# Optimization experiments

Measured on AMD Instinct MI355X. Metric: run time of the kernel, lower is better.

## Reference

```python
import jax, jax.numpy as jnp
import numpy as np

NUM_MODELS = 4
B = 16384
HIDDEN = 512
QDIM = 256
LAST_HIDDEN = 256
UW = 0.1          # uncertainty_weight
EPS = 1e-5        # LayerNorm eps (torch default)
FEAT_DIMS = [1024, 768, 512, 640]


def _linear(x, W, b):
    return x @ W.T + b


def _layernorm(h, g, b):
    mu = jnp.mean(h, axis=-1, keepdims=True)
    var = jnp.mean((h - mu) ** 2, axis=-1, keepdims=True)
    return (h - mu) * jax.lax.rsqrt(var + EPS) * g + b


def setup_inputs() -> dict:
    key = jax.random.key(0)
    ks = jax.random.split(key, 40)
    inp = {}
    for i, d in enumerate(FEAT_DIMS):
        inp[f"feat{i}"] = jax.random.normal(ks[i], (B, d), jnp.float32)
        inp[f"W_intra{i}"] = jax.random.normal(ks[4 + i], (HIDDEN, d), jnp.float32) / np.sqrt(d)
        inp[f"b_intra{i}"] = jnp.zeros((HIDDEN,), jnp.float32)
    inp["pred_scores"] = jax.random.uniform(ks[8], (B, NUM_MODELS), jnp.float32)
    inp["pred_vars"] = jax.random.uniform(ks[9], (B, NUM_MODELS), jnp.float32)
    inp["ln_g"] = jnp.ones((HIDDEN,), jnp.float32)
    inp["ln_b"] = jnp.zeros((HIDDEN,), jnp.float32)
    inp["Wq"] = jax.random.normal(ks[10], (QDIM, HIDDEN), jnp.float32) / np.sqrt(HIDDEN)
    inp["bq"] = jnp.zeros((QDIM,), jnp.float32)
    inp["Wk"] = jax.random.normal(ks[11], (QDIM, HIDDEN), jnp.float32) / np.sqrt(HIDDEN)
    inp["bk"] = jnp.zeros((QDIM,), jnp.float32)
    inp["Wv"] = jax.random.normal(ks[12], (QDIM, HIDDEN), jnp.float32) / np.sqrt(HIDDEN)
    inp["bv"] = jnp.zeros((QDIM,), jnp.float32)
    d1 = NUM_MODELS * QDIM + NUM_MODELS
    inp["W1"] = jax.random.normal(ks[13], (LAST_HIDDEN, d1), jnp.float32) / np.sqrt(d1)
    inp["b1"] = jnp.zeros((LAST_HIDDEN,), jnp.float32)
    inp["Wfc"] = jax.random.normal(ks[14], (1, LAST_HIDDEN), jnp.float32) / np.sqrt(LAST_HIDDEN)
    inp["bfc"] = jnp.zeros((1,), jnp.float32)
    return inp


def _forward(feats, pred_scores, pred_vars, W_intras, b_intras,
             ln_g, ln_b, Wq, bq, Wk, bk, Wv, bv, W1, b1, Wfc, bfc):
    # per-model branch: Linear -> ReLU -> (dropout=id) -> ReLU -> LayerNorm
    hiddens = []
    for i in range(NUM_MODELS):
        h = jax.nn.relu(_linear(feats[i], W_intras[i], b_intras[i]))
        h = jax.nn.relu(h)  # second relu after dropout (identity in eval)
        hiddens.append(_layernorm(h, ln_g, ln_b))
    H = jnp.stack(hiddens, axis=1)  # (B, M, HIDDEN)

    # cross-attention with uncertainty; NOTE source bug: key = drop(q) => keys == queries
    q = jnp.einsum('bmh,qh->bmq', H, Wq) + bq          # (B, M, Q)
    k = q                                              # faithful to `key = self.drop(q)`
    v = jnp.einsum('bmh,qh->bmq', H, Wv) + bv          # (B, M, Q)

    scores = jnp.einsum('biq,bjq->bij', q, k)          # (B, M, M)
    vars_ = pred_vars[:, None, :] + pred_vars[:, :, None]  # vars[b,i,j] = v[b,j] + v[b,i]
    scores = jax.nn.softmax(scores - UW * vars_, axis=-1)
    z = jnp.einsum('bij,bjq->biq', scores, v).reshape(B, NUM_MODELS * QDIM)

    out = jnp.concatenate([z, pred_scores], axis=-1)
    out = _linear(out, W1, b1)
    logits = _linear(out, Wfc, bfc)
    return jax.nn.sigmoid(logits)  # (B, 1)


def reference(feat0, feat1, feat2, feat3,
              W_intra0, b_intra0, W_intra1, b_intra1,
              W_intra2, b_intra2, W_intra3, b_intra3,
              pred_scores, pred_vars, ln_g, ln_b,
              Wq, bq, Wk, bk, Wv, bv, W1, b1, Wfc, bfc):
    feats = [feat0, feat1, feat2, feat3]
    W_intras = [W_intra0, W_intra1, W_intra2, W_intra3]
    b_intras = [b_intra0, b_intra1, b_intra2, b_intra3]
    return _forward(feats, pred_scores, pred_vars, W_intras, b_intras,
                    ln_g, ln_b, Wq, bq, Wk, bk, Wv, bv, W1, b1, Wfc, bfc)
```

## Files before the change

kernel.cpp:

```cpp
#include <hip/hip_runtime.h>
#include <hip/hip_bf16.h>


typedef __bf16 bf16;
typedef __bf16 bf16x4_t __attribute__((ext_vector_type(4)));
typedef __bf16 bf16x8_t __attribute__((ext_vector_type(8)));
typedef float  f32x4_t  __attribute__((ext_vector_type(4)));

__device__ __forceinline__ bf16x8_t cvt8(f32x4_t a, f32x4_t b) {
  bf16x8_t r;
  r[0] = (bf16)a[0]; r[1] = (bf16)a[1]; r[2] = (bf16)a[2]; r[3] = (bf16)a[3];
  r[4] = (bf16)b[0]; r[5] = (bf16)b[1]; r[6] = (bf16)b[2]; r[7] = (bf16)b[3];
  return r;
}

__device__ __forceinline__ void gl_lds16(const void* g, void* l) {
  __builtin_amdgcn_global_load_lds(
      (const __attribute__((address_space(1))) void*)g,
      (__attribute__((address_space(3))) void*)l, 16, 0, 0);
}

__device__ __forceinline__ bf16x8_t frag_read(const bf16* Ts, int row, int c0) {
  const int byte = row * 64 + ((c0 ^ ((row >> 1) & 3)) << 4);
  return *(const bf16x8_t*)((const char*)Ts + byte);
}

__device__ __forceinline__ void stage_b16(const bf16* __restrict__ src, int ld,
                                          int k0, bf16* lds) {
  const int l = threadIdx.x & 63;
  const int w = threadIdx.x >> 6;
#pragma unroll
  for (int j = 0; j < 2; ++j) {
    const int rb = w * 32 + j * 16;
    const int r  = rb + (l >> 2);
    const int sc = (l & 3) ^ ((r >> 1) & 3);
    gl_lds16(src + (size_t)r * ld + k0 + sc * 8, (char*)lds + rb * 64);
  }
}

__device__ __forceinline__ void commit2(const f32x4_t v[4], bf16* lds,
                                        int srow, int shalf) {
  const int sw = (srow >> 1) & 3;
  *(bf16x8_t*)((char*)lds + srow * 64 + (((shalf * 2)     ^ sw) << 4)) = cvt8(v[0], v[1]);
  *(bf16x8_t*)((char*)lds + srow * 64 + (((shalf * 2 + 1) ^ sw) << 4)) = cvt8(v[2], v[3]);
}

__device__ __forceinline__ void mfma_step(const bf16* As, const bf16* Bs,
                                          f32x4_t acc[4][4]) {
  const int lane = threadIdx.x & 63;
  const int wid  = threadIdx.x >> 6;
  const int wm = wid >> 1, wn = wid & 1;
  const int fr = lane & 15, c0 = lane >> 4;
  bf16x8_t ar[4], br[4];
#pragma unroll
  for (int mi = 0; mi < 4; ++mi) ar[mi] = frag_read(As, wm * 64 + mi * 16 + fr, c0);
#pragma unroll
  for (int ni = 0; ni < 4; ++ni) br[ni] = frag_read(Bs, wn * 64 + ni * 16 + fr, c0);
#pragma unroll
  for (int mi = 0; mi < 4; ++mi)
#pragma unroll
    for (int ni = 0; ni < 4; ++ni)
      acc[mi][ni] = __builtin_amdgcn_mfma_f32_16x16x32_bf16(ar[mi], br[ni], acc[mi][ni], 0, 0, 0);
}

#define WAIT_VM6()  asm volatile("s_waitcnt vmcnt(6)" ::: "memory")
#define WAIT_VM0()  asm volatile("s_waitcnt vmcnt(0)" ::: "memory")
#define WAIT_LGKM() asm volatile("s_waitcnt lgkmcnt(0)" ::: "memory")
#define SBAR()      __builtin_amdgcn_s_barrier()
#define SCHED0()    __builtin_amdgcn_sched_barrier(0)

template<int REG_IS_A>
__device__ __forceinline__ void core_db(
    const float* __restrict__ regsrc, int rld,
    const bf16* __restrict__ dmasrc, int dld, int K,
    bf16* R0, bf16* R1, bf16* D0, bf16* D1, f32x4_t acc[4][4])
{
  const int tid  = threadIdx.x;
  const int srow = tid >> 1, shalf = tid & 1;
  const float* Rf = regsrc + (size_t)srow * rld + shalf * 16;

  f32x4_t ra[4], rb[4];
#pragma unroll
  for (int i = 0; i < 4; ++i) ra[i] = *(const f32x4_t*)(Rf + i * 4);
  stage_b16(dmasrc, dld, 0, D0);

  for (int k0 = 0; k0 < K; k0 += 64) {
    stage_b16(dmasrc, dld, k0 + 32, D1);
#pragma unroll
    for (int i = 0; i < 4; ++i) rb[i] = *(const f32x4_t*)(Rf + k0 + 32 + i * 4);
    WAIT_VM6();
    commit2(ra, R0, srow, shalf);
    WAIT_LGKM();
    SBAR(); SCHED0();
    if (REG_IS_A) mfma_step(R0, D0, acc); else mfma_step(D0, R0, acc);
    SCHED0(); SBAR();
    if (k0 + 64 < K) {
      stage_b16(dmasrc, dld, k0 + 64, D0);
#pragma unroll
      for (int i = 0; i < 4; ++i) ra[i] = *(const f32x4_t*)(Rf + k0 + 64 + i * 4);
      WAIT_VM6();
    } else {
      WAIT_VM0();
    }
    commit2(rb, R1, srow, shalf);
    WAIT_LGKM();
    SBAR(); SCHED0();
    if (REG_IS_A) mfma_step(R1, D1, acc); else mfma_step(D1, R1, acc);
    SCHED0(); SBAR();
  }
}

template<int RELU>
__device__ __forceinline__ void epi_bf16(f32x4_t acc[4][4], bf16* __restrict__ C, int ldc,
                                         const float* __restrict__ bias) {
  const int lane = threadIdx.x & 63;
  const int wid  = threadIdx.x >> 6;
  const int wm = wid >> 1, wn = wid & 1;
  const int fr = lane & 15;
  const int rb = wm * 64 + 4 * (lane >> 4);
  const int cb = wn * 64 + fr;
  float bv[4];
#pragma unroll
  for (int ni = 0; ni < 4; ++ni) bv[ni] = bias[cb + ni * 16];
#pragma unroll
  for (int mi = 0; mi < 4; ++mi)
#pragma unroll
    for (int j = 0; j < 4; ++j)
#pragma unroll
      for (int ni = 0; ni < 4; ++ni) {
        float val = acc[mi][ni][j] + bv[ni];
        if (RELU) val = fmaxf(val, 0.f);
        C[(size_t)(rb + mi * 16 + j) * ldc + cb + ni * 16] = (bf16)val;
      }
}

__device__ __forceinline__ void cp8(bf16* d, const float* s) {
  f32x4_t x0 = *(const f32x4_t*)s;
  f32x4_t x1 = *(const f32x4_t*)(s + 4);
  *(bf16x8_t*)d = cvt8(x0, x1);
}

__global__ __launch_bounds__(256) void prep_kernel(
    const float* __restrict__ w0, const float* __restrict__ w1s,
    const float* __restrict__ w2, const float* __restrict__ w3,
    bf16* __restrict__ o0, bf16* __restrict__ o1,
    bf16* __restrict__ o2, bf16* __restrict__ o3) {
  const int t = blockIdx.x * 256 + threadIdx.x;
  if (t < 65536)       { size_t i = (size_t)t * 8;            cp8(o0 + i, w0 + i); }
  else if (t < 114688) { size_t i = (size_t)(t - 65536) * 8;  cp8(o1 + i, w1s + i); }
  else if (t < 147456) { size_t i = (size_t)(t - 114688) * 8; cp8(o2 + i, w2 + i); }
  else                 { size_t i = (size_t)(t - 147456) * 8; cp8(o3 + i, w3 + i); }
}

__global__ __launch_bounds__(256) void intra_kernel(
    const float* __restrict__ f0, const float* __restrict__ f1,
    const float* __restrict__ f2, const float* __restrict__ f3,
    const bf16* __restrict__ wb0, const bf16* __restrict__ wb1,
    const bf16* __restrict__ wb2, const bf16* __restrict__ wb3,
    const float* __restrict__ bb0, const float* __restrict__ bb1,
    const float* __restrict__ bb2, const float* __restrict__ bb3,
    bf16* __restrict__ hbuf) {
  __shared__ bf16 A0[128 * 32], A1[128 * 32], B0[128 * 32], B1[128 * 32];
  const int bid = blockIdx.x;
  const int lid = (bid & 7) * 256 + (bid >> 3);
  const int x = lid & 3;
  const int g = lid >> 2;
  const int z = g & 3;
  const int y = g >> 2;
  const float* fp; const bf16* wp; const float* bp; int K;
  switch (z) {
    case 0:  fp = f0; wp = wb0; bp = bb0; K = 1024; break;
    case 1:  fp = f1; wp = wb1; bp = bb1; K = 768;  break;
    case 2:  fp = f2; wp = wb2; bp = bb2; K = 512;  break;
    default: fp = f3; wp = wb3; bp = bb3; K = 640;  break;
  }
  f32x4_t acc[4][4];
#pragma unroll
  for (int i = 0; i < 4; ++i)
#pragma unroll
    for (int j = 0; j < 4; ++j) acc[i][j] = (f32x4_t){0.f, 0.f, 0.f, 0.f};
  core_db<1>(fp + (size_t)(y * 128) * K, K,
             wp + (size_t)(x * 128) * K, K, K, A0, A1, B0, B1, acc);
  bf16* C = hbuf + (size_t)(y * 128) * 2048 + z * 512 + x * 128;
  epi_bf16<1>(acc, C, 2048, bp + x * 128);
}

__global__ __launch_bounds__(256) void qv_kernel(
    const bf16* __restrict__ H, const float* __restrict__ Wq,
    const float* __restrict__ Wv, const float* __restrict__ bq,
    const float* __restrict__ bv, bf16* __restrict__ qvout) {
  __shared__ bf16 A0[128 * 32], A1[128 * 32], B0[128 * 32], B1[128 * 32];
  const int bid = blockIdx.x;
  const int lid = (bid & 7) * 256 + (bid >> 3);
  const int x = lid & 3, y = lid >> 2;
  const float* Wsrc = (x < 2) ? Wq : Wv;
  f32x4_t acc[4][4];
#pragma unroll
  for (int i = 0; i < 4; ++i)
#pragma unroll
    for (int j = 0; j < 4; ++j) acc[i][j] = (f32x4_t){0.f, 0.f, 0.f, 0.f};
  core_db<0>(Wsrc + (size_t)((x & 1) * 128) * 512, 512,
             H + (size_t)(y * 128) * 512, 512, 512, B0, B1, A0, A1, acc);
  const float* bias = (x < 2) ? bq + x * 128 : bv + (x - 2) * 128;
  epi_bf16<0>(acc, qvout + (size_t)(y * 128) * 512 + x * 128, 512, bias);
}

__global__ __launch_bounds__(256) void w1_kernel(
    const bf16* __restrict__ zb, const float* __restrict__ W1,
    const float* __restrict__ b1, const float* __restrict__ ps,
    float* __restrict__ obuf) {
  __shared__ bf16 A0[128 * 32], A1[128 * 32], B0[128 * 32], B1[128 * 32];
  const int bid = blockIdx.x;
  const int lid = (bid & 7) * 32 + (bid >> 3);
  const int x = lid & 1, y = lid >> 1;
  f32x4_t acc[4][4];
#pragma unroll
  for (int i = 0; i < 4; ++i)
#pragma unroll
    for (int j = 0; j < 4; ++j) acc[i][j] = (f32x4_t){0.f, 0.f, 0.f, 0.f};
  core_db<0>(W1 + (size_t)(x * 128) * 1028, 1028,
             zb + (size_t)(y * 128) * 1024, 1024, 1024, B0, B1, A0, A1, acc);

  const int lane = threadIdx.x & 63;
  const int wid  = threadIdx.x >> 6;
  const int wm = wid >> 1, wn = wid & 1;
  const int fr = lane & 15;
  const int rb = wm * 64 + 4 * (lane >> 4);
  const int cb = x * 128 + wn * 64 + fr;
  float bv[4], wt[4][4];
#pragma unroll
  for (int ni = 0; ni < 4; ++ni) {
    bv[ni] = b1[cb + ni * 16];
#pragma unroll
    for (int m = 0; m < 4; ++m) wt[ni][m] = W1[(size_t)(cb + ni * 16) * 1028 + 1024 + m];
  }
#pragma unroll
  for (int mi = 0; mi < 4; ++mi)
#pragma unroll
    for (int j = 0; j < 4; ++j) {
      const int r = y * 128 + rb + mi * 16 + j;
      f32x4_t psv = *(const f32x4_t*)(ps + (size_t)r * 4);
#pragma unroll
      for (int ni = 0; ni < 4; ++ni) {
        float val = acc[mi][ni][j] + bv[ni]
                  + psv[0] * wt[ni][0] + psv[1] * wt[ni][1]
                  + psv[2] * wt[ni][2] + psv[3] * wt[ni][3];
        obuf[(size_t)r * 256 + cb + ni * 16] = val;
      }
    }
}

__global__ __launch_bounds__(256)
void ln_kernel(bf16* __restrict__ h, const float* __restrict__ g,
               const float* __restrict__ bta) {
  const int row  = blockIdx.x * 4 + (threadIdx.x >> 6);
  const int lane = threadIdx.x & 63;
  bf16* p = h + (size_t)row * 512 + lane * 8;
  const bf16x8_t x = *(const bf16x8_t*)p;
  float xf[8]; float s = 0.f, s2 = 0.f;
#pragma unroll
  for (int j = 0; j < 8; ++j) { xf[j] = (float)x[j]; s += xf[j]; s2 += xf[j] * xf[j]; }
#pragma unroll
  for (int off = 1; off < 64; off <<= 1) { s += __shfl_xor(s, off); s2 += __shfl_xor(s2, off); }
  const float mu  = s * (1.f / 512.f);
  const float var = s2 * (1.f / 512.f) - mu * mu;
  const float inv = rsqrtf(var + 1e-5f);
  f32x4_t g0 = *(const f32x4_t*)(g + lane * 8);
  f32x4_t g1 = *(const f32x4_t*)(g + lane * 8 + 4);
  f32x4_t b0 = *(const f32x4_t*)(bta + lane * 8);
  f32x4_t b1 = *(const f32x4_t*)(bta + lane * 8 + 4);
  bf16x8_t o;
#pragma unroll
  for (int j = 0; j < 4; ++j) o[j]     = (bf16)((xf[j] - mu) * inv * g0[j] + b0[j]);
#pragma unroll
  for (int j = 0; j < 4; ++j) o[4 + j] = (bf16)((xf[4 + j] - mu) * inv * g1[j] + b1[j]);
  *(bf16x8_t*)p = o;
}

__global__ __launch_bounds__(256)
void attn_kernel(const bf16* __restrict__ qv, const float* __restrict__ pvars,
                 bf16* __restrict__ z) {
  const int b    = blockIdx.x * 4 + (threadIdx.x >> 6);
  const int lane = threadIdx.x & 63;
  float qf[4][4], vf[4][4];
#pragma unroll
  for (int i = 0; i < 4; ++i) {
    const bf16* row = qv + ((size_t)b * 4 + i) * 512;
    bf16x4_t qq = *(const bf16x4_t*)(row + lane * 4);
    bf16x4_t vv = *(const bf16x4_t*)(row + 256 + lane * 4);
#pragma unroll
    for (int c = 0; c < 4; ++c) { qf[i][c] = (float)qq[c]; vf[i][c] = (float)vv[c]; }
  }
  float s[4][4];
#pragma unroll
  for (int i = 0; i < 4; ++i)
#pragma unroll
    for (int j = 0; j < 4; ++j)
      s[i][j] = qf[i][0] * qf[j][0] + qf[i][1] * qf[j][1] + qf[i][2] * qf[j][2] + qf[i][3] * qf[j][3];
#pragma unroll
  for (int off = 1; off < 64; off <<= 1)
#pragma unroll
    for (int i = 0; i < 4; ++i)
#pragma unroll
      for (int j = 0; j < 4; ++j) s[i][j] += __shfl_xor(s[i][j], off);

  float var4[4];
#pragma unroll
  for (int m = 0; m < 4; ++m) var4[m] = pvars[(size_t)b * 4 + m];
  float w[4][4];
#pragma unroll
  for (int i = 0; i < 4; ++i) {
    float t[4]; float mx = -1e30f;
#pragma unroll
    for (int j = 0; j < 4; ++j) { t[j] = s[i][j] - 0.1f * (var4[i] + var4[j]); mx = fmaxf(mx, t[j]); }
    float sum = 0.f;
#pragma unroll
    for (int j = 0; j < 4; ++j) { t[j] = expf(t[j] - mx); sum += t[j]; }
    const float is = 1.f / sum;
#pragma unroll
    for (int j = 0; j < 4; ++j) w[i][j] = t[j] * is;
  }
#pragma unroll
  for (int i = 0; i < 4; ++i) {
    bf16x4_t zo;
#pragma unroll
    for (int c = 0; c < 4; ++c) {
      float zf = w[i][0] * vf[0][c] + w[i][1] * vf[1][c] + w[i][2] * vf[2][c] + w[i][3] * vf[3][c];
      zo[c] = (bf16)zf;
    }
    *(bf16x4_t*)(z + ((size_t)b * 4 + i) * 256 + lane * 4) = zo;
  }
}

__global__ __launch_bounds__(256)
void fc_kernel(const float* __restrict__ o, const float* __restrict__ wfc,
               const float* __restrict__ bfc, float* __restrict__ out) {
  const int b    = blockIdx.x * 4 + (threadIdx.x >> 6);
  const int lane = threadIdx.x & 63;
  f32x4_t ov = *(const f32x4_t*)(o + (size_t)b * 256 + lane * 4);
  f32x4_t wv = *(const f32x4_t*)(wfc + lane * 4);
  float p = ov[0] * wv[0] + ov[1] * wv[1] + ov[2] * wv[2] + ov[3] * wv[3];
#pragma unroll
  for (int off = 1; off < 64; off <<= 1) p += __shfl_xor(p, off);
  if (lane == 0) {
    const float lg = p + bfc[0];
    out[b] = 1.f / (1.f + expf(-lg));
  }
}

extern "C" void kernel_launch(void* const* d_in, const int* in_sizes, int n_in,
                              void* d_out, int out_size, void* d_ws, size_t ws_size,
                              hipStream_t stream) {
  (void)in_sizes; (void)n_in; (void)out_size; (void)ws_size;
  const float* feat[4] = {(const float*)d_in[0], (const float*)d_in[3],
                          (const float*)d_in[6], (const float*)d_in[9]};
  const float* Wi[4]   = {(const float*)d_in[1], (const float*)d_in[4],
                          (const float*)d_in[7], (const float*)d_in[10]};
  const float* bi[4]   = {(const float*)d_in[2], (const float*)d_in[5],
                          (const float*)d_in[8], (const float*)d_in[11]};
  const float* ps  = (const float*)d_in[12];
  const float* pv  = (const float*)d_in[13];
  const float* lng = (const float*)d_in[14];
  const float* lnb = (const float*)d_in[15];
  const float* Wq  = (const float*)d_in[16];
  const float* bq  = (const float*)d_in[17];
  const float* Wv  = (const float*)d_in[20];
  const float* bvp = (const float*)d_in[21];
  const float* W1  = (const float*)d_in[22];
  const float* b1  = (const float*)d_in[23];
  const float* Wfc = (const float*)d_in[24];
  const float* bfc = (const float*)d_in[25];

  char* ws = (char*)d_ws;
  const size_t MB = 1024 * 1024;
  bf16*  hbuf  = (bf16*)ws;
  bf16*  zbuf  = (bf16*)ws;
  float* obuf  = (float*)(ws + 32 * MB);
  bf16*  wb0   = (bf16*)(ws + 64 * MB);
  bf16*  wb1   = (bf16*)(ws + 65 * MB);
  bf16*  wb2   = (bf16*)(ws + 65 * MB + 786432);
  bf16*  wb3   = (bf16*)(ws + 66 * MB + 262144);
  bf16*  qvout = (bf16*)(ws + 64 * MB);

  hipLaunchKernelGGL(prep_kernel, dim3(736), dim3(256), 0, stream,
                     Wi[0], Wi[1], Wi[2], Wi[3], wb0, wb1, wb2, wb3);
  hipLaunchKernelGGL(intra_kernel, dim3(2048), dim3(256), 0, stream,
                     feat[0], feat[1], feat[2], feat[3],
                     wb0, wb1, wb2, wb3, bi[0], bi[1], bi[2], bi[3], hbuf);
  hipLaunchKernelGGL(ln_kernel, dim3(65536 / 4), dim3(256), 0, stream, hbuf, lng, lnb);
  hipLaunchKernelGGL(qv_kernel, dim3(2048), dim3(256), 0, stream,
                     hbuf, Wq, Wv, bq, bvp, qvout);
  hipLaunchKernelGGL(attn_kernel, dim3(16384 / 4), dim3(256), 0, stream, qvout, pv, zbuf);
  hipLaunchKernelGGL(w1_kernel, dim3(256), dim3(256), 0, stream, zbuf, W1, b1, ps, obuf);
  hipLaunchKernelGGL(fc_kernel, dim3(16384 / 4), dim3(256), 0, stream, obuf, Wfc, bfc, (float*)d_out);
}
```

Baseline: 279.4 us.

## Fuse LayerNorm into per-model intra GEMM with full-row 64x512 tiles

Reshapes the intra-branch GEMM so each block computes a 64-row by full 512-column tile, with each warp covering 128 columns. This lets bias, ReLU and LayerNorm be applied in LDS right after the GEMM, so the separate ln_kernel launch and its read-modify-write pass over the hidden buffer go away. The cost is a much larger LDS footprint (72KB), more accumulator registers per thread, and halved grid size, which lowers occupancy and latency hiding.

```diff
diff --git a/kernel.cpp b/kernel.cpp
--- a/kernel.cpp
+++ b/kernel.cpp
@@ -38,6 +38,19 @@
   }
 }
 
+__device__ __forceinline__ void stage_b512(const bf16* __restrict__ src, int ld,
+                                           int k0, bf16* lds) {
+  const int l = threadIdx.x & 63;
+  const int w = threadIdx.x >> 6;
+#pragma unroll
+  for (int j = 0; j < 8; ++j) {
+    const int rb = w * 128 + j * 16;
+    const int r  = rb + (l >> 2);
+    const int sc = (l & 3) ^ ((r >> 1) & 3);
+    gl_lds16(src + (size_t)r * ld + k0 + sc * 8, (char*)lds + rb * 64);
+  }
+}
+
 __device__ __forceinline__ void commit2(const f32x4_t v[4], bf16* lds,
                                         int srow, int shalf) {
   const int sw = (srow >> 1) & 3;
@@ -63,7 +76,25 @@
       acc[mi][ni] = __builtin_amdgcn_mfma_f32_16x16x32_bf16(ar[mi], br[ni], acc[mi][ni], 0, 0, 0);
 }
 
+__device__ __forceinline__ void mfma_step8(const bf16* As, const bf16* Bs,
+                                           f32x4_t acc[4][8]) {
+  const int lane = threadIdx.x & 63;
+  const int wn   = threadIdx.x >> 6;
+  const int fr = lane & 15, c0 = lane >> 4;
+  bf16x8_t ar[4], br[8];
+#pragma unroll
+  for (int mi = 0; mi < 4; ++mi) ar[mi] = frag_read(As, mi * 16 + fr, c0);
+#pragma unroll
+  for (int ni = 0; ni < 8; ++ni) br[ni] = frag_read(Bs, wn * 128 + ni * 16 + fr, c0);
+#pragma unroll
+  for (int mi = 0; mi < 4; ++mi)
+#pragma unroll
+    for (int ni = 0; ni < 8; ++ni)
+      acc[mi][ni] = __builtin_amdgcn_mfma_f32_16x16x32_bf16(ar[mi], br[ni], acc[mi][ni], 0, 0, 0);
+}
+
 #define WAIT_VM6()  asm volatile("s_waitcnt vmcnt(6)" ::: "memory")
+#define WAIT_VM10() asm volatile("s_waitcnt vmcnt(10)" ::: "memory")
 #define WAIT_VM0()  asm volatile("s_waitcnt vmcnt(0)" ::: "memory")
 #define WAIT_LGKM() asm volatile("s_waitcnt lgkmcnt(0)" ::: "memory")
 #define SBAR()      __builtin_amdgcn_s_barrier()
@@ -152,21 +183,26 @@
   else                 { size_t i = (size_t)(t - 147456) * 8; cp8(o3 + i, w3 + i); }
 }
 
-__global__ __launch_bounds__(256) void intra_kernel(
+__global__ __launch_bounds__(256, 2) void intra_ln_kernel(
     const float* __restrict__ f0, const float* __restrict__ f1,
     const float* __restrict__ f2, const float* __restrict__ f3,
     const bf16* __restrict__ wb0, const bf16* __restrict__ wb1,
     const bf16* __restrict__ wb2, const bf16* __restrict__ wb3,
     const float* __restrict__ bb0, const float* __restrict__ bb1,
     const float* __restrict__ bb2, const float* __restrict__ bb3,
-    bf16* __restrict__ hbuf) {
-  __shared__ bf16 A0[128 * 32], A1[128 * 32], B0[128 * 32], B1[128 * 32];
+    const float* __restrict__ lng, const float* __restrict__ lnb,
+    bf16* __restrict__ Hout) {
+  __shared__ __align__(16) char smem[73728];
+  bf16* B0 = (bf16*)smem;
+  bf16* B1 = (bf16*)(smem + 32768);
+  bf16* A0 = (bf16*)(smem + 65536);
+  bf16* A1 = (bf16*)(smem + 69632);
+  bf16* hl = (bf16*)smem;
+
   const int bid = blockIdx.x;
-  const int lid = (bid & 7) * 256 + (bid >> 3);
-  const int x = lid & 3;
-  const int g = lid >> 2;
-  const int z = g & 3;
-  const int y = g >> 2;
+  const int lid = (bid & 7) * 128 + (bid >> 3);
+  const int z = lid & 3;
+  const int y = lid >> 2;
   const float* fp; const bf16* wp; const float* bp; int K;
   switch (z) {
     case 0:  fp = f0; wp = wb0; bp = bb0; K = 1024; break;
@@ -174,15 +210,89 @@
     case 2:  fp = f2; wp = wb2; bp = bb2; K = 512;  break;
     default: fp = f3; wp = wb3; bp = bb3; K = 640;  break;
   }
-  f32x4_t acc[4][4];
+  const int tid  = threadIdx.x;
+  const int lane = tid & 63;
+  const int wn   = tid >> 6;
+  const int srow = tid >> 2, sq = tid & 3;
+  const float* Af = fp + (size_t)(y * 64 + srow) * K + sq * 8;
+  const int abyte = srow * 64 + ((sq ^ ((srow >> 1) & 3)) << 4);
+
+  f32x4_t acc[4][8];
 #pragma unroll
   for (int i = 0; i < 4; ++i)
 #pragma unroll
-    for (int j = 0; j < 4; ++j) acc[i][j] = (f32x4_t){0.f, 0.f, 0.f, 0.f};
-  core_db<1>(fp + (size_t)(y * 128) * K, K,
-             wp + (size_t)(x * 128) * K, K, K, A0, A1, B0, B1, acc);
-  bf16* C = hbuf + (size_t)(y * 128) * 2048 + z * 512 + x * 128;
-  epi_bf16<1>(acc, C, 2048, bp + x * 128);
+    for (int j = 0; j < 8; ++j) acc[i][j] = (f32x4_t){0.f, 0.f, 0.f, 0.f};
+
+  f32x4_t ra0, ra1, rb0, rb1;
+  ra0 = *(const f32x4_t*)(Af + 0);  ra1 = *(const f32x4_t*)(Af + 4);
+  stage_b512(wp, K, 0, B0);
+
+  for (int k0 = 0; k0 < K; k0 += 64) {
+    stage_b512(wp, K, k0 + 32, B1);
+    rb0 = *(const f32x4_t*)(Af + k0 + 32);  rb1 = *(const f32x4_t*)(Af + k0 + 36);
+    WAIT_VM10();
+    { f32x4_t v[1]; (void)v; }
+    *(bf16x8_t*)((char*)A0 + abyte) = cvt8(ra0, ra1);
+    WAIT_LGKM();
+    SBAR(); SCHED0();
+    mfma_step8(A0, B0, acc);
+    SCHED0(); SBAR();
+    if (k0 + 64 < K) {
+      stage_b512(wp, K, k0 + 64, B0);
+      ra0 = *(const f32x4_t*)(Af + k0 + 64);  ra1 = *(const f32x4_t*)(Af + k0 + 68);
+      WAIT_VM10();
+    } else {
+      WAIT_VM0();
+    }
+    *(bf16x8_t*)((char*)A1 + abyte) = cvt8(rb0, rb1);
+    WAIT_LGKM();
+    SBAR(); SCHED0();
+    mfma_step8(A1, B1, acc);
+    SCHED0(); SBAR();
+  }
+
+  const int fr = lane & 15;
+  const int rbase = 4 * (lane >> 4);
+  const int cb = wn * 128 + fr;
+  float bv[8];
+#pragma unroll
+  for (int ni = 0; ni < 8; ++ni) bv[ni] = bp[cb + ni * 16];
+#pragma unroll
+  for (int mi = 0; mi < 4; ++mi)
+#pragma unroll
+    for (int j = 0; j < 4; ++j) {
+      const int row = mi * 16 + rbase + j;
+#pragma unroll
+      for (int ni = 0; ni < 8; ++ni) {
+        float v = fmaxf(acc[mi][ni][j] + bv[ni], 0.f);
+        hl[row * 512 + cb + ni * 16] = (bf16)v;
+      }
+    }
+  __syncthreads();
+
+  f32x4_t g0 = *(const f32x4_t*)(lng + lane * 8);
+  f32x4_t g1 = *(const f32x4_t*)(lng + lane * 8 + 4);
+  f32x4_t be0 = *(const f32x4_t*)(lnb + lane * 8);
+  f32x4_t be1 = *(const f32x4_t*)(lnb + lane * 8 + 4);
+#pragma unroll
+  for (int r16 = 0; r16 < 16; ++r16) {
+    const int row = wn * 16 + r16;
+    const bf16x8_t xv = *(const bf16x8_t*)(hl + row * 512 + lane * 8);
+    float xf[8]; float s = 0.f, s2 = 0.f;
+#pragma unroll
+    for (int j = 0; j < 8; ++j) { xf[j] = (float)xv[j]; s += xf[j]; s2 += xf[j] * xf[j]; }
+#pragma unroll
+    for (int off = 1; off < 64; off <<= 1) { s += __shfl_xor(s, off); s2 += __shfl_xor(s2, off); }
+    const float mu  = s * (1.f / 512.f);
+    const float var = s2 * (1.f / 512.f) - mu * mu;
+    const float inv = rsqrtf(var + 1e-5f);
+    bf16x8_t o;
+#pragma unroll
+    for (int j = 0; j < 4; ++j) o[j]     = (bf16)((xf[j] - mu) * inv * g0[j] + be0[j]);
+#pragma unroll
+    for (int j = 0; j < 4; ++j) o[4 + j] = (bf16)((xf[4 + j] - mu) * inv * g1[j] + be1[j]);
+    *(bf16x8_t*)(Hout + (size_t)(y * 64 + row) * 2048 + z * 512 + lane * 8) = o;
+  }
 }
 
 __global__ __launch_bounds__(256) void qv_kernel(
@@ -248,33 +358,6 @@
         obuf[(size_t)r * 256 + cb + ni * 16] = val;
       }
     }
-}
-
-__global__ __launch_bounds__(256)
-void ln_kernel(bf16* __restrict__ h, const float* __restrict__ g,
-               const float* __restrict__ bta) {
-  const int row  = blockIdx.x * 4 + (threadIdx.x >> 6);
-  const int lane = threadIdx.x & 63;
-  bf16* p = h + (size_t)row * 512 + lane * 8;
-  const bf16x8_t x = *(const bf16x8_t*)p;
-  float xf[8]; float s = 0.f, s2 = 0.f;
-#pragma unroll
-  for (int j = 0; j < 8; ++j) { xf[j] = (float)x[j]; s += xf[j]; s2 += xf[j] * xf[j]; }
-#pragma unroll
-  for (int off = 1; off < 64; off <<= 1) { s += __shfl_xor(s, off); s2 += __shfl_xor(s2, off); }
-  const float mu  = s * (1.f / 512.f);
-  const float var = s2 * (1.f / 512.f) - mu * mu;
-  const float inv = rsqrtf(var + 1e-5f);
-  f32x4_t g0 = *(const f32x4_t*)(g + lane * 8);
-  f32x4_t g1 = *(const f32x4_t*)(g + lane * 8 + 4);
-  f32x4_t b0 = *(const f32x4_t*)(bta + lane * 8);
-  f32x4_t b1 = *(const f32x4_t*)(bta + lane * 8 + 4);
-  bf16x8_t o;
-#pragma unroll
-  for (int j = 0; j < 4; ++j) o[j]     = (bf16)((xf[j] - mu) * inv * g0[j] + b0[j]);
-#pragma unroll
-  for (int j = 0; j < 4; ++j) o[4 + j] = (bf16)((xf[4 + j] - mu) * inv * g1[j] + b1[j]);
-  *(bf16x8_t*)p = o;
 }
 
 __global__ __launch_bounds__(256)
@@ -373,7 +456,7 @@
 
   char* ws = (char*)d_ws;
   const size_t MB = 1024 * 1024;
-  bf16*  hbuf  = (bf16*)ws;
+  bf16*  Hbuf  = (bf16*)ws;
   bf16*  zbuf  = (bf16*)ws;
   float* obuf  = (float*)(ws + 32 * MB);
   bf16*  wb0   = (bf16*)(ws + 64 * MB);
@@ -384,12 +467,12 @@
 
   hipLaunchKernelGGL(prep_kernel, dim3(736), dim3(256), 0, stream,
                      Wi[0], Wi[1], Wi[2], Wi[3], wb0, wb1, wb2, wb3);
-  hipLaunchKernelGGL(intra_kernel, dim3(2048), dim3(256), 0, stream,
+  hipLaunchKernelGGL(intra_ln_kernel, dim3(1024), dim3(256), 0, stream,
                      feat[0], feat[1], feat[2], feat[3],
-                     wb0, wb1, wb2, wb3, bi[0], bi[1], bi[2], bi[3], hbuf);
-  hipLaunchKernelGGL(ln_kernel, dim3(65536 / 4), dim3(256), 0, stream, hbuf, lng, lnb);
+                     wb0, wb1, wb2, wb3, bi[0], bi[1], bi[2], bi[3],
+                     lng, lnb, Hbuf);
   hipLaunchKernelGGL(qv_kernel, dim3(2048), dim3(256), 0, stream,
-                     hbuf, Wq, Wv, bq, bvp, qvout);
+                     Hbuf, Wq, Wv, bq, bvp, qvout);
   hipLaunchKernelGGL(attn_kernel, dim3(16384 / 4), dim3(256), 0, stream, qvout, pv, zbuf);
   hipLaunchKernelGGL(w1_kernel, dim3(256), dim3(256), 0, stream, zbuf, W1, b1, ps, obuf);
   hipLaunchKernelGGL(fc_kernel, dim3(16384 / 4), dim3(256), 0, stream, obuf, Wfc, bfc, (float*)d_out);
```

Measured after the change: 255.4 us. 1.09x faster.

## Stage fp32 operands via LDS DMA with triple-buffered GEMM pipeline

Applied to the files above, without the earlier changes.

Replaces the register-staged fp32 operand path (global load to registers, convert, write to LDS) with direct global-to-LDS DMA of fp32 tiles in a swizzled layout. The fp32-to-bf16 conversion now happens at fragment-read time. The two-stage double buffer becomes a three-deep ring buffer with graded vmcnt waits and raised wave priority around the MFMA block, so more loads are in flight and VGPR staging is removed. This costs 72KB of LDS per block, which likely lowers occupancy to one or two blocks per CU, and doubles LDS read traffic for the fp32 operand.

```diff
diff --git a/kernel.cpp b/kernel.cpp
--- a/kernel.cpp
+++ b/kernel.cpp
@@ -20,11 +20,13 @@
       (__attribute__((address_space(3))) void*)l, 16, 0, 0);
 }
 
-__device__ __forceinline__ bf16x8_t frag_read(const bf16* Ts, int row, int c0) {
+#define SBAR()   __builtin_amdgcn_s_barrier()
+#define SCHED0() __builtin_amdgcn_sched_barrier(0)
+
+__device__ __forceinline__ bf16x8_t frag_b16(const bf16* Ts, int row, int c0) {
   const int byte = row * 64 + ((c0 ^ ((row >> 1) & 3)) << 4);
   return *(const bf16x8_t*)((const char*)Ts + byte);
 }
-
 __device__ __forceinline__ void stage_b16(const bf16* __restrict__ src, int ld,
                                           int k0, bf16* lds) {
   const int l = threadIdx.x & 63;
@@ -38,24 +40,60 @@
   }
 }
 
-__device__ __forceinline__ void commit2(const f32x4_t v[4], bf16* lds,
-                                        int srow, int shalf) {
-  const int sw = (srow >> 1) & 3;
-  *(bf16x8_t*)((char*)lds + srow * 64 + (((shalf * 2)     ^ sw) << 4)) = cvt8(v[0], v[1]);
-  *(bf16x8_t*)((char*)lds + srow * 64 + (((shalf * 2 + 1) ^ sw) << 4)) = cvt8(v[2], v[3]);
-}
-
-__device__ __forceinline__ void mfma_step(const bf16* As, const bf16* Bs,
-                                          f32x4_t acc[4][4]) {
+__device__ __forceinline__ bf16x8_t frag_f32(const float* Ts, int row, int g) {
+  const int p0 = (2 * g)     ^ (row & 7);
+  const int p1 = (2 * g + 1) ^ (row & 7);
+  f32x4_t lo = *(const f32x4_t*)((const char*)Ts + row * 128 + (p0 << 4));
+  f32x4_t hi = *(const f32x4_t*)((const char*)Ts + row * 128 + (p1 << 4));
+  return cvt8(lo, hi);
+}
+__device__ __forceinline__ void stage_f32(const float* __restrict__ src, int ld,
+                                          int k0, float* lds) {
+  const int l = threadIdx.x & 63;
+  const int w = threadIdx.x >> 6;
+#pragma unroll
+  for (int j = 0; j < 4; ++j) {
+    const int rb = w * 32 + j * 8;
+    const int r  = rb + (l >> 3);
+    const int q  = (l & 7) ^ (r & 7);
+    gl_lds16(src + (size_t)r * ld + k0 + q * 4, (char*)lds + rb * 128);
+  }
+}
+
+template<int AF32>
+__device__ __forceinline__ void stage_deep(const void* A, int lda, const void* B,
+                                           int ldb, int k0, char* buf) {
+  if (AF32) {
+    stage_f32((const float*)A, lda, k0, (float*)buf);
+    stage_b16((const bf16*)B, ldb, k0, (bf16*)(buf + 16384));
+  } else {
+    stage_b16((const bf16*)A, lda, k0, (bf16*)buf);
+    stage_f32((const float*)B, ldb, k0, (float*)(buf + 8192));
+  }
+}
+
+template<int AF32>
+__device__ __forceinline__ void mfma_deep(const char* buf, f32x4_t acc[4][4]) {
   const int lane = threadIdx.x & 63;
   const int wid  = threadIdx.x >> 6;
   const int wm = wid >> 1, wn = wid & 1;
-  const int fr = lane & 15, c0 = lane >> 4;
+  const int fr = lane & 15, g = lane >> 4;
   bf16x8_t ar[4], br[4];
-#pragma unroll
-  for (int mi = 0; mi < 4; ++mi) ar[mi] = frag_read(As, wm * 64 + mi * 16 + fr, c0);
-#pragma unroll
-  for (int ni = 0; ni < 4; ++ni) br[ni] = frag_read(Bs, wn * 64 + ni * 16 + fr, c0);
+  if (AF32) {
+    const float* Af = (const float*)buf;
+    const bf16*  Bb = (const bf16*)(buf + 16384);
+#pragma unroll
+    for (int mi = 0; mi < 4; ++mi) ar[mi] = frag_f32(Af, wm * 64 + mi * 16 + fr, g);
+#pragma unroll
+    for (int ni = 0; ni < 4; ++ni) br[ni] = frag_b16(Bb, wn * 64 + ni * 16 + fr, g);
+  } else {
+    const bf16*  Ab = (const bf16*)buf;
+    const float* Bf = (const float*)(buf + 8192);
+#pragma unroll
+    for (int mi = 0; mi < 4; ++mi) ar[mi] = frag_b16(Ab, wm * 64 + mi * 16 + fr, g);
+#pragma unroll
+    for (int ni = 0; ni < 4; ++ni) br[ni] = frag_f32(Bf, wn * 64 + ni * 16 + fr, g);
+  }
 #pragma unroll
   for (int mi = 0; mi < 4; ++mi)
 #pragma unroll
@@ -63,50 +101,27 @@
       acc[mi][ni] = __builtin_amdgcn_mfma_f32_16x16x32_bf16(ar[mi], br[ni], acc[mi][ni], 0, 0, 0);
 }
 
-#define WAIT_VM6()  asm volatile("s_waitcnt vmcnt(6)" ::: "memory")
-#define WAIT_VM0()  asm volatile("s_waitcnt vmcnt(0)" ::: "memory")
-#define WAIT_LGKM() asm volatile("s_waitcnt lgkmcnt(0)" ::: "memory")
-#define SBAR()      __builtin_amdgcn_s_barrier()
-#define SCHED0()    __builtin_amdgcn_sched_barrier(0)
-
-template<int REG_IS_A>
-__device__ __forceinline__ void core_db(
-    const float* __restrict__ regsrc, int rld,
-    const bf16* __restrict__ dmasrc, int dld, int K,
-    bf16* R0, bf16* R1, bf16* D0, bf16* D1, f32x4_t acc[4][4])
-{
-  const int tid  = threadIdx.x;
-  const int srow = tid >> 1, shalf = tid & 1;
-  const float* Rf = regsrc + (size_t)srow * rld + shalf * 16;
-
-  f32x4_t ra[4], rb[4];
-#pragma unroll
-  for (int i = 0; i < 4; ++i) ra[i] = *(const f32x4_t*)(Rf + i * 4);
-  stage_b16(dmasrc, dld, 0, D0);
-
-  for (int k0 = 0; k0 < K; k0 += 64) {
-    stage_b16(dmasrc, dld, k0 + 32, D1);
-#pragma unroll
-    for (int i = 0; i < 4; ++i) rb[i] = *(const f32x4_t*)(Rf + k0 + 32 + i * 4);
-    WAIT_VM6();
-    commit2(ra, R0, srow, shalf);
-    WAIT_LGKM();
+template<int AF32>
+__device__ __forceinline__ void core_deep3(const void* A, int lda, const void* B,
+                                           int ldb, int K, char* lds,
+                                           f32x4_t acc[4][4]) {
+  const int nt = K >> 5;
+  stage_deep<AF32>(A, lda, B, ldb, 0,  lds);
+  stage_deep<AF32>(A, lda, B, ldb, 32, lds + 24576);
+  stage_deep<AF32>(A, lda, B, ldb, 64, lds + 49152);
+  int buf = 0;
+  for (int t = 0; t < nt; ++t) {
+    const int ahead = nt - 1 - t;
+    if (ahead >= 2)      asm volatile("s_waitcnt vmcnt(12)" ::: "memory");
+    else if (ahead == 1) asm volatile("s_waitcnt vmcnt(6)"  ::: "memory");
+    else                 asm volatile("s_waitcnt vmcnt(0)"  ::: "memory");
     SBAR(); SCHED0();
-    if (REG_IS_A) mfma_step(R0, D0, acc); else mfma_step(D0, R0, acc);
+    __builtin_amdgcn_s_setprio(1);
+    mfma_deep<AF32>(lds + buf * 24576, acc);
+    __builtin_amdgcn_s_setprio(0);
     SCHED0(); SBAR();
-    if (k0 + 64 < K) {
-      stage_b16(dmasrc, dld, k0 + 64, D0);
-#pragma unroll
-      for (int i = 0; i < 4; ++i) ra[i] = *(const f32x4_t*)(Rf + k0 + 64 + i * 4);
-      WAIT_VM6();
-    } else {
-      WAIT_VM0();
-    }
-    commit2(rb, R1, srow, shalf);
-    WAIT_LGKM();
-    SBAR(); SCHED0();
-    if (REG_IS_A) mfma_step(R1, D1, acc); else mfma_step(D1, R1, acc);
-    SCHED0(); SBAR();
+    if (t + 3 < nt) stage_deep<AF32>(A, lda, B, ldb, (t + 3) * 32, lds + buf * 24576);
+    buf = (buf == 2) ? 0 : buf + 1;
   }
 }
 
@@ -160,7 +175,7 @@
     const float* __restrict__ bb0, const float* __restrict__ bb1,
     const float* __restrict__ bb2, const float* __restrict__ bb3,
     bf16* __restrict__ hbuf) {
-  __shared__ bf16 A0[128 * 32], A1[128 * 32], B0[128 * 32], B1[128 * 32];
+  __shared__ __align__(16) char lds[73728];
   const int bid = blockIdx.x;
   const int lid = (bid & 7) * 256 + (bid >> 3);
   const int x = lid & 3;
@@ -179,75 +194,10 @@
   for (int i = 0; i < 4; ++i)
 #pragma unroll
     for (int j = 0; j < 4; ++j) acc[i][j] = (f32x4_t){0.f, 0.f, 0.f, 0.f};
-  core_db<1>(fp + (size_t)(y * 128) * K, K,
-             wp + (size_t)(x * 128) * K, K, K, A0, A1, B0, B1, acc);
+  core_deep3<1>(fp + (size_t)(y * 128) * K, K,
+                wp + (size_t)(x * 128) * K, K, K, lds, acc);
   bf16* C = hbuf + (size_t)(y * 128) * 2048 + z * 512 + x * 128;
   epi_bf16<1>(acc, C, 2048, bp + x * 128);
-}
-
-__global__ __launch_bounds__(256) void qv_kernel(
-    const bf16* __restrict__ H, const float* __restrict__ Wq,
-    const float* __restrict__ Wv, const float* __restrict__ bq,
-    const float* __restrict__ bv, bf16* __restrict__ qvout) {
-  __shared__ bf16 A0[128 * 32], A1[128 * 32], B0[128 * 32], B1[128 * 32];
-  const int bid = blockIdx.x;
-  const int lid = (bid & 7) * 256 + (bid >> 3);
-  const int x = lid & 3, y = lid >> 2;
-  const float* Wsrc = (x < 2) ? Wq : Wv;
-  f32x4_t acc[4][4];
-#pragma unroll
-  for (int i = 0; i < 4; ++i)
-#pragma unroll
-    for (int j = 0; j < 4; ++j) acc[i][j] = (f32x4_t){0.f, 0.f, 0.f, 0.f};
-  core_db<0>(Wsrc + (size_t)((x & 1) * 128) * 512, 512,
-             H + (size_t)(y * 128) * 512, 512, 512, B0, B1, A0, A1, acc);
-  const float* bias = (x < 2) ? bq + x * 128 : bv + (x - 2) * 128;
-  epi_bf16<0>(acc, qvout + (size_t)(y * 128) * 512 + x * 128, 512, bias);
-}
-
-__global__ __launch_bounds__(256) void w1_kernel(
-    const bf16* __restrict__ zb, const float* __restrict__ W1,
-    const float* __restrict__ b1, const float* __restrict__ ps,
-    float* __restrict__ obuf) {
-  __shared__ bf16 A0[128 * 32], A1[128 * 32], B0[128 * 32], B1[128 * 32];
-  const int bid = blockIdx.x;
-  const int lid = (bid & 7) * 32 + (bid >> 3);
-  const int x = lid & 1, y = lid >> 1;
-  f32x4_t acc[4][4];
-#pragma unroll
-  for (int i = 0; i < 4; ++i)
-#pragma unroll
-    for (int j = 0; j < 4; ++j) acc[i][j] = (f32x4_t){0.f, 0.f, 0.f, 0.f};
-  core_db<0>(W1 + (size_t)(x * 128) * 1028, 1028,
-             zb + (size_t)(y * 128) * 1024, 1024, 1024, B0, B1, A0, A1, acc);
-
-  const int lane = threadIdx.x & 63;
-  const int wid  = threadIdx.x >> 6;
-  const int wm = wid >> 1, wn = wid & 1;
-  const int fr = lane & 15;
-  const int rb = wm * 64 + 4 * (lane >> 4);
-  const int cb = x * 128 + wn * 64 + fr;
-  float bv[4], wt[4][4];
-#pragma unroll
-  for (int ni = 0; ni < 4; ++ni) {
-    bv[ni] = b1[cb + ni * 16];
-#pragma unroll
-    for (int m = 0; m < 4; ++m) wt[ni][m] = W1[(size_t)(cb + ni * 16) * 1028 + 1024 + m];
-  }
-#pragma unroll
-  for (int mi = 0; mi < 4; ++mi)
-#pragma unroll
-    for (int j = 0; j < 4; ++j) {
-      const int r = y * 128 + rb + mi * 16 + j;
-      f32x4_t psv = *(const f32x4_t*)(ps + (size_t)r * 4);
-#pragma unroll
-      for (int ni = 0; ni < 4; ++ni) {
-        float val = acc[mi][ni][j] + bv[ni]
-                  + psv[0] * wt[ni][0] + psv[1] * wt[ni][1]
-                  + psv[2] * wt[ni][2] + psv[3] * wt[ni][3];
-        obuf[(size_t)r * 256 + cb + ni * 16] = val;
-      }
-    }
 }
 
 __global__ __launch_bounds__(256)
@@ -275,6 +225,71 @@
 #pragma unroll
   for (int j = 0; j < 4; ++j) o[4 + j] = (bf16)((xf[4 + j] - mu) * inv * g1[j] + b1[j]);
   *(bf16x8_t*)p = o;
+}
+
+__global__ __launch_bounds__(256) void qv_kernel(
+    const bf16* __restrict__ H, const float* __restrict__ Wq,
+    const float* __restrict__ Wv, const float* __restrict__ bq,
+    const float* __restrict__ bv, bf16* __restrict__ qvout) {
+  __shared__ __align__(16) char lds[73728];
+  const int bid = blockIdx.x;
+  const int lid = (bid & 7) * 256 + (bid >> 3);
+  const int x = lid & 3, y = lid >> 2;
+  const float* Wsrc = (x < 2) ? Wq : Wv;
+  f32x4_t acc[4][4];
+#pragma unroll
+  for (int i = 0; i < 4; ++i)
+#pragma unroll
+    for (int j = 0; j < 4; ++j) acc[i][j] = (f32x4_t){0.f, 0.f, 0.f, 0.f};
+  core_deep3<0>(H + (size_t)(y * 128) * 512, 512,
+                Wsrc + (size_t)((x & 1) * 128) * 512, 512, 512, lds, acc);
+  const float* bias = (x < 2) ? bq + x * 128 : bv + (x - 2) * 128;
+  epi_bf16<0>(acc, qvout + (size_t)(y * 128) * 512 + x * 128, 512, bias);
+}
+
+__global__ __launch_bounds__(256) void w1_kernel(
+    const bf16* __restrict__ zb, const float* __restrict__ W1,
+    const float* __restrict__ b1, const float* __restrict__ ps,
+    float* __restrict__ obuf) {
+  __shared__ __align__(16) char lds[73728];
+  const int bid = blockIdx.x;
+  const int lid = (bid & 7) * 32 + (bid >> 3);
+  const int x = lid & 1, y = lid >> 1;
+  f32x4_t acc[4][4];
+#pragma unroll
+  for (int i = 0; i < 4; ++i)
+#pragma unroll
+    for (int j = 0; j < 4; ++j) acc[i][j] = (f32x4_t){0.f, 0.f, 0.f, 0.f};
+  core_deep3<0>(zb + (size_t)(y * 128) * 1024, 1024,
+                W1 + (size_t)(x * 128) * 1028, 1028, 1024, lds, acc);
+
+  const int lane = threadIdx.x & 63;
+  const int wid  = threadIdx.x >> 6;
+  const int wm = wid >> 1, wn = wid & 1;
+  const int fr = lane & 15;
+  const int rb = wm * 64 + 4 * (lane >> 4);
+  const int cb = x * 128 + wn * 64 + fr;
+  float bv[4], wt[4][4];
+#pragma unroll
+  for (int ni = 0; ni < 4; ++ni) {
+    bv[ni] = b1[cb + ni * 16];
+#pragma unroll
+    for (int m = 0; m < 4; ++m) wt[ni][m] = W1[(size_t)(cb + ni * 16) * 1028 + 1024 + m];
+  }
+#pragma unroll
+  for (int mi = 0; mi < 4; ++mi)
+#pragma unroll
+    for (int j = 0; j < 4; ++j) {
+      const int r = y * 128 + rb + mi * 16 + j;
+      f32x4_t psv = *(const f32x4_t*)(ps + (size_t)r * 4);
+#pragma unroll
+      for (int ni = 0; ni < 4; ++ni) {
+        float val = acc[mi][ni][j] + bv[ni]
+                  + psv[0] * wt[ni][0] + psv[1] * wt[ni][1]
+                  + psv[2] * wt[ni][2] + psv[3] * wt[ni][3];
+        obuf[(size_t)r * 256 + cb + ni * 16] = val;
+      }
+    }
 }
 
 __global__ __launch_bounds__(256)
```

New measurement: 256.4 us. 1.09x faster.
